# Kernel optimization log

Hardware: AMD Instinct MI355X
Metric: run time of the kernel (lower is better)

The kernel has to match this reference:

```python
import jax, jax.numpy as jnp
import numpy as np

B, T, C, NH = 2, 128, 384, 6
H = 768          # memory MLP hidden (expansion=2)
P, M = 4, 16     # persistent + long-term memory tokens; prefix_len = P+M
LR, MOM, DECAY = 0.01, 0.9, 0.001

def setup_inputs() -> dict:
    key = jax.random.key(0)
    ks = jax.random.split(key, 12)
    s = 0.02
    return {
        'x':          jax.random.normal(ks[0], (B, T, C), jnp.float32),
        'c_attn_w':   jax.random.normal(ks[1], (C, 3 * C), jnp.float32) * s,
        'c_attn_b':   jnp.zeros((3 * C,), jnp.float32),
        'c_proj_w':   jax.random.normal(ks[2], (C, C), jnp.float32) * s,
        'c_proj_b':   jnp.zeros((C,), jnp.float32),
        'ln1_g': jnp.ones((C,), jnp.float32), 'ln1_b': jnp.zeros((C,), jnp.float32),
        'ln2_g': jnp.ones((C,), jnp.float32), 'ln2_b': jnp.zeros((C,), jnp.float32),
        'fc_w':       jax.random.normal(ks[3], (C, 4 * C), jnp.float32) * s,
        'fc_b':       jnp.zeros((4 * C,), jnp.float32),
        'pr_w':       jax.random.normal(ks[4], (4 * C, C), jnp.float32) * s,
        'pr_b':       jnp.zeros((C,), jnp.float32),
        'mem_w1':     jax.random.normal(ks[5], (C, H), jnp.float32) * s,
        'mem_w2':     jax.random.normal(ks[6], (H, C), jnp.float32) * s,
        'wk':         jax.random.normal(ks[7], (C, C), jnp.float32) * s,
        'wv':         jax.random.normal(ks[8], (C, C), jnp.float32) * s,
        'mem_queries': jax.random.normal(ks[9], (M, C), jnp.float32) * s,
        'persist':    jax.random.normal(ks[10], (P, C), jnp.float32) * s,
    }

def _ln(x, g, b):
    mu = jnp.mean(x, -1, keepdims=True)
    var = jnp.mean((x - mu) ** 2, -1, keepdims=True)
    return (x - mu) * jax.lax.rsqrt(var + 1e-5) * g + b

def _scan_log(gates, tokens):
    # x[t] = gate[t]*x[t-1] + token[t] via log-cumsum trick (scan axis = 1)
    while gates.ndim < tokens.ndim:
        gates = gates[..., None]
    g = jnp.clip(gates, 1e-7, 1.0 - 1e-7)
    lc = jnp.cumsum(jnp.log(g), axis=1)
    return jnp.cumsum(tokens * jnp.exp(-lc), axis=1) * jnp.exp(lc)

def _forward(x, c_attn_w, c_attn_b, c_proj_w, c_proj_b, ln1_g, ln1_b, ln2_g, ln2_b,
             fc_w, fc_b, pr_w, pr_b, mem_w1, mem_w2, wk, wv, mem_queries, persist):
    b = x.shape[0]
    hd = C // NH
    PL = P + M
    xn = _ln(x, ln1_g, ln1_b)
    # --- retrieve long-term memory tokens with previous-segment memory weights ---
    retr = jax.nn.silu(mem_queries @ mem_w1) @ mem_w2              # [M, C]
    pref = jnp.concatenate([persist, retr], axis=0)                # [PL, C]
    seq = jnp.concatenate([jnp.broadcast_to(pref, (b, PL, C)), xn], axis=1)  # [b, t, C]
    t = seq.shape[1]
    # --- prefix-LM masked attention ---
    qkv = seq @ c_attn_w + c_attn_b
    q, k, v = jnp.split(qkv, 3, axis=-1)
    def heads(z):
        return z.reshape(b, t, NH, hd).transpose(0, 2, 1, 3)       # [b, nh, t, hd]
    q, k, v = heads(q), heads(k), heads(v)
    sc = jnp.einsum('bhqd,bhkd->bhqk', q, k) / np.float32(np.sqrt(hd))
    idx = jnp.arange(t)
    kp = idx < PL  # key in prefix
    # prefix_lm_mask: key_in_prefix OR (both in suffix AND causal)
    allowed = kp[None, :] | ((~kp[:, None]) & (~kp[None, :]) & (idx[:, None] >= idx[None, :]))
    sc = jnp.where(allowed, sc, -jnp.inf)
    y = jnp.einsum('bhqk,bhkd->bhqd', jax.nn.softmax(sc, axis=-1), v)
    y = y.transpose(0, 2, 1, 3).reshape(b, t, C) @ c_proj_w + c_proj_b
    h1 = x + y[:, PL:, :]                                          # suffix (segment) outputs
    h2n = _ln(h1, ln2_g, ln2_b)
    h2 = h1 + (jax.nn.gelu(h2n @ fc_w + fc_b) @ pr_w + pr_b)
    # --- Titans neural memory update (per-token grads + momentum/decay scans) ---
    km = xn @ wk                                                   # [b, T, C]
    vm = xn @ wv
    hh = km @ mem_w1                                               # [b, T, H]
    a = jax.nn.silu(hh)
    err = a @ mem_w2 - vm                                          # [b, T, C]
    dw2 = jnp.einsum('bth,btc->bthc', a, err)                      # [b, T, H, C]
    sg = jax.nn.sigmoid(hh)
    dh = (err @ mem_w2.T) * (sg * (1.0 + hh * (1.0 - sg)))         # silu'
    dw1 = jnp.einsum('btc,bth->btch', km, dh)                      # [b, T, C, H]
    gm = jnp.full((b, T), MOM, x.dtype)
    scale = -(LR * (1.0 - MOM))
    m1 = _scan_log(gm, scale * dw1)
    m2 = _scan_log(gm, scale * dw2)
    def upd(w0, m):  # W[t] = (1-decay)*W[t-1] + m[t], W[-1] = w0
        toks = jnp.concatenate([jnp.broadcast_to(w0, (b,) + w0.shape)[:, None], m], axis=1)
        g = jnp.concatenate([jnp.ones((b, 1), x.dtype),
                             jnp.full((b, T), 1.0 - DECAY, x.dtype)], axis=1)
        return _scan_log(g, toks)[:, -1]
    w1f = upd(mem_w1, m1)                                          # [b, C, H]
    w2f = upd(mem_w2, m2)                                          # [b, H, C]
    # --- combine block output with updated-memory retrieval ---
    mem_out = jnp.einsum('bth,bhc->btc',
                         jax.nn.silu(jnp.einsum('btc,bch->bth', h2, w1f)), w2f)
    return h2 + mem_out

def reference(x, c_attn_w, c_attn_b, c_proj_w, c_proj_b, ln1_g, ln1_b, ln2_g, ln2_b,
              fc_w, fc_b, pr_w, pr_b, mem_w1, mem_w2, wk, wv, mem_queries, persist):
    return _forward(x, c_attn_w, c_attn_b, c_proj_w, c_proj_b, ln1_g, ln1_b, ln2_g, ln2_b,
                    fc_w, fc_b, pr_w, pr_b, mem_w1, mem_w2, wk, wv, mem_queries, persist)
```

## Files before the change

### kernel.cpp

```cpp
#include <hip/hip_runtime.h>
#include <math.h>

#define B_ 2
#define T_ 128
#define Cc 384
#define NH_ 6
#define HD 64
#define Hh 768
#define P_ 4
#define M_ 16
#define PL_ 20
#define TT 148

typedef unsigned short u16;
typedef short short8 __attribute__((ext_vector_type(8)));
typedef float f32x4 __attribute__((ext_vector_type(4)));

__device__ __forceinline__ u16 f2bf(float f) {
  unsigned int u = __float_as_uint(f);
  u += 0x7FFFu + ((u >> 16) & 1u);
  return (u16)(u >> 16);
}
__device__ __forceinline__ float siluf(float v) { return v / (1.f + expf(-v)); }
__device__ __forceinline__ float geluf(float v) {
  float x3 = v*v*v;
  return 0.5f*v*(1.f + tanhf(0.7978845608028654f*(v + 0.044715f*x3)));
}
template<int ACT> __device__ __forceinline__ float act_apply(float v) {
  if (ACT == 1) return geluf(v);
  if (ACT == 2) return siluf(v);
  return v;
}
__device__ __forceinline__ float coef_f(int k) {
  float e = (float)(T_ - k);
  return (exp2f(e * -0.00144342f) - exp2f(e * -0.15200310f)) * (1.0f/0.099f);
}
__device__ __forceinline__ void st_tr4(u16* dst, float v0, float v1, float v2, float v3) {
  union { u16 u[4]; uint2 d; } q;
  q.u[0]=f2bf(v0); q.u[1]=f2bf(v1); q.u[2]=f2bf(v2); q.u[3]=f2bf(v3);
  *(uint2*)dst = q.d;
}
__device__ __forceinline__ float wave_sum(float s) {
  #pragma unroll
  for (int off = 32; off; off >>= 1) s += __shfl_xor(s, off);
  return s;
}

struct Prm {
  const float *x,*c_attn_w,*c_attn_b,*c_proj_w,*c_proj_b,*ln1_g,*ln1_b,*ln2_g,*ln2_b,
              *fc_w,*fc_b,*pr_w,*pr_b,*mem_w1,*mem_w2,*wk,*wv,*mem_q,*persist;
  float *qkv,*vmb,*h1,*h2,*hhb,*outp;
  u16 *cattnT,*cprojT,*wkT,*wvT,*fcT,*prT,*w1tr,*w2tr,*w2pl,*memq,*hid,*seqb,*yb,*h2n,
      *fco,*h2b,*kmb,*kmTc,*ab,*abTc,*errB,*errT,*dhT,*w1fT,*w2fT,*ub;
  float scale, dpow;
};

template<int KSTEPS>
__device__ __forceinline__ void mfma_core(const u16* __restrict__ A,
    const u16* __restrict__ BT, int M, int mBase, int nBase, float (*red)[64][36])
{
  const long K = (long)KSTEPS * 128;
  int l = threadIdx.x & 63, w = threadIdx.x >> 6;
  int lr = l & 15, kg = l >> 4;
  long r0 = (long)min(mBase + lr, M - 1);
  long r1 = (long)min(mBase + 16 + lr, M - 1);
  long c0 = nBase + lr;
  long ko = (long)w * KSTEPS * 32 + kg * 8;
  const u16* pa0 = A + r0*K + ko;
  const u16* pa1 = A + r1*K + ko;
  const u16* pb0 = BT + c0*K + ko;
  const u16* pb1 = BT + (c0+16)*K + ko;
  const u16* pb2 = BT + (c0+32)*K + ko;
  const u16* pb3 = BT + (c0+48)*K + ko;
  f32x4 acc[2][4] = {};
  short8 a0 = *(const short8*)pa0, a1 = *(const short8*)pa1;
  short8 b0 = *(const short8*)pb0, b1 = *(const short8*)pb1;
  short8 b2 = *(const short8*)pb2, b3 = *(const short8*)pb3;
  #pragma unroll
  for (int t = 0; t < KSTEPS; ++t) {
    short8 xa0=a0, xa1=a1, xb0=b0, xb1=b1, xb2=b2, xb3=b3;
    if (t+1 < KSTEPS) {
      int o = (t+1)*32;
      a0 = *(const short8*)(pa0+o); a1 = *(const short8*)(pa1+o);
      b0 = *(const short8*)(pb0+o); b1 = *(const short8*)(pb1+o);
      b2 = *(const short8*)(pb2+o); b3 = *(const short8*)(pb3+o);
    }
    acc[0][0] = __builtin_amdgcn_mfma_f32_16x16x32_bf16(xa0, xb0, acc[0][0], 0,0,0);
    acc[0][1] = __builtin_amdgcn_mfma_f32_16x16x32_bf16(xa0, xb1, acc[0][1], 0,0,0);
    acc[0][2] = __builtin_amdgcn_mfma_f32_16x16x32_bf16(xa0, xb2, acc[0][2], 0,0,0);
    acc[0][3] = __builtin_amdgcn_mfma_f32_16x16x32_bf16(xa0, xb3, acc[0][3], 0,0,0);
    acc[1][0] = __builtin_amdgcn_mfma_f32_16x16x32_bf16(xa1, xb0, acc[1][0], 0,0,0);
    acc[1][1] = __builtin_amdgcn_mfma_f32_16x16x32_bf16(xa1, xb1, acc[1][1], 0,0,0);
    acc[1][2] = __builtin_amdgcn_mfma_f32_16x16x32_bf16(xa1, xb2, acc[1][2], 0,0,0);
    acc[1][3] = __builtin_amdgcn_mfma_f32_16x16x32_bf16(xa1, xb3, acc[1][3], 0,0,0);
  }
  #pragma unroll
  for (int i = 0; i < 2; ++i)
    #pragma unroll
    for (int j = 0; j < 4; ++j)
      *(f32x4*)&red[w][j*16 + lr][i*16 + kg*4] = acc[i][j];
  __syncthreads();
}

__device__ __forceinline__ void reduce8(float (*red)[64][36], float v[8], int& row0, int& col) {
  int tid = threadIdx.x;
  col = tid & 63;
  row0 = (tid >> 6) * 8;
  #pragma unroll
  for (int q = 0; q < 2; ++q) {
    f32x4 s = *(f32x4*)&red[0][col][row0 + q*4];
    s += *(f32x4*)&red[1][col][row0 + q*4];
    s += *(f32x4*)&red[2][col][row0 + q*4];
    s += *(f32x4*)&red[3][col][row0 + q*4];
    v[q*4+0] = s[0]; v[q*4+1] = s[1]; v[q*4+2] = s[2]; v[q*4+3] = s[3];
  }
}

template<int KSTEPS, int ACT, bool BIAS, bool RES, bool STF, bool STB, bool STTR>
__device__ __forceinline__ void gemm_task(const u16* A, const u16* BT,
    const float* bias, const float* res, float rscale,
    float* outF, u16* outB, u16* outT, int M, int N,
    int xx, int yy, float (*red)[64][36])
{
  int mBase = yy*32, nBase = xx*64;
  mfma_core<KSTEPS>(A, BT, M, mBase, nBase, red);
  float v[8]; int row0, col;
  reduce8(red, v, row0, col);
  int c = nBase + col;
  float bv = BIAS ? bias[c] : 0.f;
  #pragma unroll
  for (int q = 0; q < 8; ++q) {
    int r = mBase + row0 + q;
    float val = act_apply<ACT>(v[q] + bv);
    if (RES && r < M) val += rscale * res[(long)r*N + c];
    v[q] = val;
    if (r < M) {
      if (STF) outF[(long)r*N + c] = val;
      if (STB) outB[(long)r*N + c] = f2bf(val);
    }
  }
  if (STTR) {
    #pragma unroll
    for (int q = 0; q < 2; ++q) {
      int r = mBase + row0 + q*4;
      if (r < M) {
        int zz = r >> 7, t0 = r & 127;
        st_tr4(&outT[((long)zz*N + c)*128 + t0], v[q*4], v[q*4+1], v[q*4+2], v[q*4+3]);
      }
    }
  }
}

__global__ __launch_bounds__(256)
void k0_prep(Prm p)
{
  __shared__ float lds[1056];
  const int t = blockIdx.x;
  const int tid = threadIdx.x, w = tid >> 6, lane = tid & 63;
  if (t < 2592) {
    const float* src; u16* dst; int K, N, tile;
    int b = t;
    if (b < 432)       { src=p.c_attn_w; dst=p.cattnT; K=384;  N=1152; tile=b; }
    else if (b < 576)  { src=p.c_proj_w; dst=p.cprojT; K=384;  N=384;  tile=b-432; }
    else if (b < 720)  { src=p.wk;       dst=p.wkT;    K=384;  N=384;  tile=b-576; }
    else if (b < 864)  { src=p.wv;       dst=p.wvT;    K=384;  N=384;  tile=b-720; }
    else if (b < 1440) { src=p.fc_w;     dst=p.fcT;    K=384;  N=1536; tile=b-864; }
    else if (b < 2016) { src=p.pr_w;     dst=p.prT;    K=1536; N=384;  tile=b-1440; }
    else if (b < 2304) { src=p.mem_w1;   dst=p.w1tr;   K=384;  N=768;  tile=b-2016; }
    else               { src=p.mem_w2;   dst=p.w2tr;   K=768;  N=384;  tile=b-2304; }
    int ntx = N >> 5;
    int n0 = (tile % ntx) << 5, k0 = (tile / ntx) << 5;
    float (*fl)[33] = reinterpret_cast<float(*)[33]>(lds);
    int tr = tid >> 3, tc4 = (tid & 7) << 2;
    float4 vv = *(const float4*)&src[(long)(k0 + tr)*N + n0 + tc4];
    fl[tr][tc4] = vv.x; fl[tr][tc4+1] = vv.y; fl[tr][tc4+2] = vv.z; fl[tr][tc4+3] = vv.w;
    __syncthreads();
    st_tr4(&dst[(long)(n0 + tr)*K + k0 + tc4],
           fl[tc4][tr], fl[tc4+1][tr], fl[tc4+2][tr], fl[tc4+3][tr]);
  } else if (t < 2888) {
    int i = (t - 2592)*256 + tid;
    if (i < 73728) {
      float4 v = *(const float4*)&p.mem_w2[(long)i*4];
      st_tr4(&p.w2pl[(long)i*4], v.x, v.y, v.z, v.w);
    } else if (i < 73728 + 1536) {
      int j = i - 73728;
      float4 v = *(const float4*)&p.mem_q[(long)j*4];
      st_tr4(&p.memq[(long)j*4], v.x, v.y, v.z, v.w);
    } else if (i < 73728 + 1536 + 384) {
      int j = i - 73728 - 1536;
      float4 v = *(const float4*)&p.persist[(long)j*4];
      st_tr4(&p.seqb[(long)j*4], v.x, v.y, v.z, v.w);
      st_tr4(&p.seqb[(long)TT*384 + j*4], v.x, v.y, v.z, v.w);
    }
  } else {
    int row = (t - 2888)*4 + w;
    const float* src = p.x + (long)row*384;
    float v[6];
    #pragma unroll
    for (int i = 0; i < 6; ++i) v[i] = src[lane + i*64];
    float mu = wave_sum(v[0]+v[1]+v[2]+v[3]+v[4]+v[5]) * (1.f/384.f);
    float sq = 0.f;
    #pragma unroll
    for (int i = 0; i < 6; ++i) { float d = v[i]-mu; sq += d*d; }
    float rstd = rsqrtf(wave_sum(sq)*(1.f/384.f) + 1e-5f);
    u16* dst = p.seqb + ((long)(row >> 7)*TT + PL_ + (row & 127))*384;
    #pragma unroll
    for (int i = 0; i < 6; ++i) {
      int cc = lane + i*64;
      dst[cc] = f2bf((v[i]-mu)*rstd*p.ln1_g[cc] + p.ln1_b[cc]);
    }
  }
}

__global__ __launch_bounds__(256, 2)
void k0b_hid(Prm p)
{
  __shared__ float red[4][64][36];
  gemm_task<3,2,false,false,false,true,false>(p.memq, p.w1tr, nullptr, nullptr, 0.f,
      nullptr, p.hid, nullptr, 16, 768, blockIdx.x, 0, red);
}

__global__ __launch_bounds__(256, 2)
void k0c_retr(Prm p)
{
  __shared__ float red[4][64][36];
  int nBase = blockIdx.x*64;
  mfma_core<6>(p.hid, p.w2tr, 16, 0, nBase, red);
  float v[8]; int row0, col;
  reduce8(red, v, row0, col);
  int c = nBase + col;
  #pragma unroll
  for (int q = 0; q < 8; ++q) {
    int r = row0 + q;
    if (r < 16) {
      u16 bv = f2bf(v[q]);
      p.seqb[(long)(P_ + r)*384 + c] = bv;
      p.seqb[(long)(TT + P_ + r)*384 + c] = bv;
    }
  }
}

__global__ __launch_bounds__(256, 2)
void k1_qkv(Prm p)
{
  __shared__ float red[4][64][36];
  int t = blockIdx.x;
  int xx = t % 30, yy = t / 30;
  int nb = xx * 64;
  const u16* BT; int n0, seg;
  if (nb < 1152)      { BT = p.cattnT; n0 = nb;        seg = 0; }
  else if (nb < 1536) { BT = p.wkT;    n0 = nb - 1152; seg = 1; }
  else                { BT = p.wvT;    n0 = nb - 1536; seg = 2; }
  int mBase = yy*32;
  mfma_core<3>(p.seqb, BT, 296, mBase, n0, red);
  float v[8]; int row0, col;
  reduce8(red, v, row0, col);
  int c = n0 + col;
  if (seg == 0) {
    float bv = p.c_attn_b[c];
    #pragma unroll
    for (int q = 0; q < 8; ++q) {
      int r = mBase + row0 + q;
      if (r < 296) p.qkv[(long)r*1152 + c] = v[q] + bv;
    }
  } else if (seg == 1) {
    #pragma unroll
    for (int q = 0; q < 8; ++q) {
      int r = mBase + row0 + q;
      if (r < 296) {
        int z = r/148, tt2 = r - 20 - z*148;
        if (tt2 >= 0) p.kmb[((long)z*128 + tt2)*384 + c] = f2bf(v[q]);
      }
    }
    #pragma unroll
    for (int q = 0; q < 2; ++q) {
      int r = mBase + row0 + q*4;
      if (r < 296) {
        int z = r/148, t0 = r - 20 - z*148;
        if (t0 >= 0)
          st_tr4(&p.kmTc[((long)z*384 + c)*128 + t0],
                 v[q*4]*coef_f(t0), v[q*4+1]*coef_f(t0+1),
                 v[q*4+2]*coef_f(t0+2), v[q*4+3]*coef_f(t0+3));
      }
    }
  } else {
    #pragma unroll
    for (int q = 0; q < 8; ++q) {
      int r = mBase + row0 + q;
      if (r < 296) {
        int z = r/148, tt2 = r - 20 - z*148;
        if (tt2 >= 0) p.vmb[((long)z*128 + tt2)*384 + c] = v[q];
      }
    }
  }
}

__global__ __launch_bounds__(256)
void k2_attn(Prm p)
{
  __shared__ float qs4[4][64];
  __shared__ float pp4[4][152];
  const int tid = threadIdx.x, w = tid >> 6, lane = tid & 63;
  int t = blockIdx.x*4 + w;
  int qr = PL_ + (t & 127);
  int h  = (t >> 7) % 6;
  int b  = (t / 768) & 1;
  const float* base = p.qkv + (long)b*TT*1152;
  float* qs = qs4[w];
  float* pp = pp4[w];
  qs[lane] = base[(long)qr*1152 + h*64 + lane];
  float mloc = -1e30f;
  for (int k = lane; k < TT; k += 64) {
    float s = -1e30f;
    if (k <= qr) {
      const float* kp = base + (long)k*1152 + 384 + h*64;
      float acc = 0.f;
      #pragma unroll
      for (int d = 0; d < 64; ++d) acc += qs[d]*kp[d];
      s = acc * 0.125f;
    }
    pp[k] = s;
    mloc = fmaxf(mloc, s);
  }
  #pragma unroll
  for (int off = 32; off; off >>= 1) mloc = fmaxf(mloc, __shfl_xor(mloc, off));
  float ssum = 0.f;
  for (int k = lane; k < TT; k += 64) {
    float e = (k <= qr) ? expf(pp[k] - mloc) : 0.f;
    pp[k] = e; ssum += e;
  }
  ssum = wave_sum(ssum);
  float inv = 1.f / ssum;
  float acc = 0.f;
  const float* vb = base + 768 + h*64 + lane;
  int k = 0;
  for (; k + 4 <= qr + 1; k += 4)
    acc += pp[k]*vb[(long)k*1152] + pp[k+1]*vb[(long)(k+1)*1152]
         + pp[k+2]*vb[(long)(k+2)*1152] + pp[k+3]*vb[(long)(k+3)*1152];
  for (; k <= qr; ++k) acc += pp[k]*vb[(long)k*1152];
  p.yb[((long)b*128 + (t & 127))*384 + h*64 + lane] = f2bf(acc * inv);
}

__global__ __launch_bounds__(256, 2)
void k3_h1hh(Prm p)
{
  __shared__ float red[4][64][36];
  int t = blockIdx.x;
  if (t < 48) {
    gemm_task<3,0,true,true,true,false,false>(p.yb, p.cprojT, p.c_proj_b, p.x, 1.f,
        p.h1, nullptr, nullptr, 256, 384, t % 6, t / 6, red);
  } else {
    int tt2 = t - 48;
    int xx = tt2 % 12, yy = tt2 / 12;
    int mBase = yy*32, nBase = xx*64;
    mfma_core<3>(p.kmb, p.w1tr, 256, mBase, nBase, red);
    float v[8]; int row0, col;
    reduce8(red, v, row0, col);
    int c = nBase + col;
    float s8[8];
    #pragma unroll
    for (int q = 0; q < 8; ++q) {
      int r = mBase + row0 + q;
      p.hhb[(long)r*768 + c] = v[q];
      s8[q] = siluf(v[q]);
      p.ab[(long)r*768 + c] = f2bf(s8[q]);
    }
    #pragma unroll
    for (int q = 0; q < 2; ++q) {
      int r = mBase + row0 + q*4;
      int zz = r >> 7, t0 = r & 127;
      st_tr4(&p.abTc[((long)zz*768 + c)*128 + t0],
             s8[q*4]*coef_f(t0), s8[q*4+1]*coef_f(t0+1),
             s8[q*4+2]*coef_f(t0+2), s8[q*4+3]*coef_f(t0+3));
    }
  }
}

__global__ __launch_bounds__(256, 2)
void k4_ln2err(Prm p)
{
  __shared__ float red[4][64][36];
  int t = blockIdx.x;
  const int tid = threadIdx.x, w = tid >> 6, lane = tid & 63;
  if (t < 64) {
    int row = t*4 + w;
    const float* src = p.h1 + (long)row*384;
    float v[6];
    #pragma unroll
    for (int i = 0; i < 6; ++i) v[i] = src[lane + i*64];
    float mu = wave_sum(v[0]+v[1]+v[2]+v[3]+v[4]+v[5]) * (1.f/384.f);
    float sq = 0.f;
    #pragma unroll
    for (int i = 0; i < 6; ++i) { float d = v[i]-mu; sq += d*d; }
    float rstd = rsqrtf(wave_sum(sq)*(1.f/384.f) + 1e-5f);
    u16* dst = p.h2n + (long)row*384;
    #pragma unroll
    for (int i = 0; i < 6; ++i) {
      int cc = lane + i*64;
      dst[cc] = f2bf((v[i]-mu)*rstd*p.ln2_g[cc] + p.ln2_b[cc]);
    }
  } else {
    int tt2 = t - 64;
    gemm_task<6,0,false,true,false,true,true>(p.ab, p.w2tr, nullptr, p.vmb, -1.f,
        nullptr, p.errB, p.errT, 256, 384, tt2 % 6, tt2 / 6, red);
  }
}

__global__ __launch_bounds__(256, 2)
void k5_fcodh(Prm p)
{
  __shared__ float red[4][64][36];
  int t = blockIdx.x;
  if (t < 192) {
    gemm_task<3,1,true,false,false,true,false>(p.h2n, p.fcT, p.fc_b, nullptr, 0.f,
        nullptr, p.fco, nullptr, 256, 1536, t % 24, t / 24, red);
  } else {
    int tt2 = t - 192;
    int xx = tt2 % 12, yy = tt2 / 12;
    int mBase = yy*32, nBase = xx*64;
    mfma_core<3>(p.errB, p.w2pl, 256, mBase, nBase, red);
    float v[8]; int row0, col;
    reduce8(red, v, row0, col);
    int c = nBase + col;
    #pragma unroll
    for (int q = 0; q < 8; ++q) {
      int r = mBase + row0 + q;
      float h = p.hhb[(long)r*768 + c];
      float sg = 1.f/(1.f + expf(-h));
      v[q] = v[q] * (sg*(1.f + h*(1.f - sg)));
    }
    #pragma unroll
    for (int q = 0; q < 2; ++q) {
      int r = mBase + row0 + q*4;
      int zz = r >> 7, t0 = r & 127;
      st_tr4(&p.dhT[((long)zz*768 + c)*128 + t0], v[q*4], v[q*4+1], v[q*4+2], v[q*4+3]);
    }
  }
}

__global__ __launch_bounds__(256, 2)
void k6_h2wupd(Prm p)
{
  __shared__ float red[4][64][36];
  int t = blockIdx.x;
  if (t < 48) {
    gemm_task<12,0,true,true,true,true,false>(p.fco, p.prT, p.pr_b, p.h1, 1.f,
        p.h2, p.h2b, nullptr, 256, 384, t % 6, t / 6, red);
  } else {
    const u16 *A, *BT; const float* W0; u16* Oz; int M, N, xx, yy, z;
    if (t < 336) {
      int tt2 = t - 48;
      xx = tt2 % 12; yy = (tt2 / 12) % 12; z = tt2 / 144;
      M = 384; N = 768;
      A = p.kmTc + (long)z*M*128; BT = p.dhT + (long)z*N*128;
      W0 = p.mem_w1; Oz = p.w1fT + (long)z*M*N;
    } else {
      int tt2 = t - 336;
      xx = tt2 % 6; yy = (tt2 / 6) % 24; z = tt2 / 144;
      M = 768; N = 384;
      A = p.abTc + (long)z*M*128; BT = p.errT + (long)z*N*128;
      W0 = p.mem_w2; Oz = p.w2fT + (long)z*M*N;
    }
    int mBase = yy*32, nBase = xx*64;
    mfma_core<1>(A, BT, M, mBase, nBase, red);
    float v[8]; int row0, col;
    reduce8(red, v, row0, col);
    int c = nBase + col;
    #pragma unroll
    for (int q = 0; q < 8; ++q) {
      int r = mBase + row0 + q;
      v[q] = p.dpow*W0[(long)r*N + c] + p.scale*v[q];
    }
    int r0 = mBase + row0;
    st_tr4(&Oz[(long)c*M + r0],     v[0], v[1], v[2], v[3]);
    st_tr4(&Oz[(long)c*M + r0 + 4], v[4], v[5], v[6], v[7]);
  }
}

__global__ __launch_bounds__(256, 2)
void k7_ub(Prm p)
{
  __shared__ float red[4][64][36];
  int t = blockIdx.x;
  int z = t / 48, rr = t % 48;
  gemm_task<3,2,false,false,false,true,false>(
      p.h2b + (long)z*128*384, p.w1fT + (long)z*768*384, nullptr, nullptr, 0.f,
      nullptr, p.ub + (long)z*128*768, nullptr, 128, 768, rr % 12, rr / 12, red);
}

__global__ __launch_bounds__(256, 2)
void k8_out(Prm p)
{
  __shared__ float red[4][64][36];
  int t = blockIdx.x;
  int z = t / 24, rr = t % 24;
  gemm_task<6,0,false,true,true,false,false>(
      p.ub + (long)z*128*768, p.w2fT + (long)z*384*768, nullptr,
      p.h2 + (long)z*128*384, 1.f,
      p.outp + (long)z*128*384, nullptr, nullptr, 128, 384, rr % 6, rr / 6, red);
}

extern "C" void kernel_launch(void* const* d_in, const int* in_sizes, int n_in,
                              void* d_out, int out_size, void* d_ws, size_t ws_size,
                              hipStream_t stream)
{
  Prm p;
  p.x        = (const float*)d_in[0];
  p.c_attn_w = (const float*)d_in[1];
  p.c_attn_b = (const float*)d_in[2];
  p.c_proj_w = (const float*)d_in[3];
  p.c_proj_b = (const float*)d_in[4];
  p.ln1_g    = (const float*)d_in[5];
  p.ln1_b    = (const float*)d_in[6];
  p.ln2_g    = (const float*)d_in[7];
  p.ln2_b    = (const float*)d_in[8];
  p.fc_w     = (const float*)d_in[9];
  p.fc_b     = (const float*)d_in[10];
  p.pr_w     = (const float*)d_in[11];
  p.pr_b     = (const float*)d_in[12];
  p.mem_w1   = (const float*)d_in[13];
  p.mem_w2   = (const float*)d_in[14];
  p.wk       = (const float*)d_in[15];
  p.wv       = (const float*)d_in[16];
  p.mem_q    = (const float*)d_in[17];
  p.persist  = (const float*)d_in[18];

  float* f = (float*)d_ws;
  p.qkv = f;            f += 296L*1152;
  p.vmb = f;            f += 256L*384;
  p.h1  = f;            f += 256L*384;
  p.h2  = f;            f += 256L*384;
  p.hhb = f;            f += 256L*768;
  u16* b = (u16*)f;
  p.cattnT = b;  b += 1152L*384;
  p.cprojT = b;  b += 384L*384;
  p.wkT    = b;  b += 384L*384;
  p.wvT    = b;  b += 384L*384;
  p.fcT    = b;  b += 1536L*384;
  p.prT    = b;  b += 384L*1536;
  p.w1tr   = b;  b += 768L*384;
  p.w2tr   = b;  b += 384L*768;
  p.w2pl   = b;  b += 768L*384;
  p.memq   = b;  b += 16L*384;
  p.hid    = b;  b += 16L*768;
  p.seqb   = b;  b += 2L*TT*384;
  p.yb     = b;  b += 256L*384;
  p.h2n    = b;  b += 256L*384;
  p.fco    = b;  b += 256L*1536;
  p.h2b    = b;  b += 256L*384;
  p.kmb    = b;  b += 256L*384;
  p.kmTc   = b;  b += 2L*384*128;
  p.ab     = b;  b += 256L*768;
  p.abTc   = b;  b += 2L*768*128;
  p.errB   = b;  b += 256L*384;
  p.errT   = b;  b += 2L*384*128;
  p.dhT    = b;  b += 2L*768*128;
  p.w1fT   = b;  b += 2L*768*384;
  p.w2fT   = b;  b += 2L*384*768;
  p.ub     = b;  b += 2L*128*768;
  p.outp   = (float*)d_out;
  p.dpow   = powf(0.999f, 128.f);
  p.scale  = -0.001f;

  hipLaunchKernelGGL(k0_prep,   dim3(2952), dim3(256), 0, stream, p);
  hipLaunchKernelGGL(k0b_hid,   dim3(12),   dim3(256), 0, stream, p);
  hipLaunchKernelGGL(k0c_retr,  dim3(6),    dim3(256), 0, stream, p);
  hipLaunchKernelGGL(k1_qkv,    dim3(300),  dim3(256), 0, stream, p);
  hipLaunchKernelGGL(k2_attn,   dim3(384),  dim3(256), 0, stream, p);
  hipLaunchKernelGGL(k3_h1hh,   dim3(144),  dim3(256), 0, stream, p);
  hipLaunchKernelGGL(k4_ln2err, dim3(112),  dim3(256), 0, stream, p);
  hipLaunchKernelGGL(k5_fcodh,  dim3(288),  dim3(256), 0, stream, p);
  hipLaunchKernelGGL(k6_h2wupd, dim3(624),  dim3(256), 0, stream, p);
  hipLaunchKernelGGL(k7_ub,     dim3(96),   dim3(256), 0, stream, p);
  hipLaunchKernelGGL(k8_out,    dim3(48),   dim3(256), 0, stream, p);
}
```

Baseline: 99.04 us.

## Regroup independent stages into fewer launches and fuse memory hidden into retrieval

The kernel that computes the memory-query hidden layer is folded into the retrieval kernel. Each of its 6 blocks recomputes the full 16x768 hidden activation into LDS, which removes one launch and a global round trip. The later stages are regrouped so that independent work shares a launch: attention runs with the hh GEMM, c_proj with the error GEMM, LN2 with dh, and fc with the weight updates. The final h2 projection gets its own small launch. This drops one launch and its barrier and gives small GEMMs more co-resident work, at the cost of redundant hidden computation, lower occupancy in the retrieval kernel, and mixed block types within a launch.

Result: slower. 123.5 us (+24.7%).

```diff
diff --git a/kernel.cpp b/kernel.cpp
--- a/kernel.cpp
+++ b/kernel.cpp
@@ -50,7 +50,7 @@
   const float *x,*c_attn_w,*c_attn_b,*c_proj_w,*c_proj_b,*ln1_g,*ln1_b,*ln2_g,*ln2_b,
               *fc_w,*fc_b,*pr_w,*pr_b,*mem_w1,*mem_w2,*wk,*wv,*mem_q,*persist;
   float *qkv,*vmb,*h1,*h2,*hhb,*outp;
-  u16 *cattnT,*cprojT,*wkT,*wvT,*fcT,*prT,*w1tr,*w2tr,*w2pl,*memq,*hid,*seqb,*yb,*h2n,
+  u16 *cattnT,*cprojT,*wkT,*wvT,*fcT,*prT,*w1tr,*w2tr,*w2pl,*memq,*seqb,*yb,*h2n,
       *fco,*h2b,*kmb,*kmTc,*ab,*abTc,*errB,*errT,*dhT,*w1fT,*w2fT,*ub;
   float scale, dpow;
 };
@@ -212,20 +212,25 @@
   }
 }
 
-__global__ __launch_bounds__(256, 2)
-void k0b_hid(Prm p)
-{
-  __shared__ float red[4][64][36];
-  gemm_task<3,2,false,false,false,true,false>(p.memq, p.w1tr, nullptr, nullptr, 0.f,
-      nullptr, p.hid, nullptr, 16, 768, blockIdx.x, 0, red);
-}
-
-__global__ __launch_bounds__(256, 2)
+__global__ __launch_bounds__(256, 1)
 void k0c_retr(Prm p)
 {
   __shared__ float red[4][64][36];
+  __shared__ u16 hidl[16*768];
+  for (int xx = 0; xx < 12; ++xx) {
+    mfma_core<3>(p.memq, p.w1tr, 16, 0, xx*64, red);
+    float v[8]; int row0, col;
+    reduce8(red, v, row0, col);
+    int c = xx*64 + col;
+    #pragma unroll
+    for (int q = 0; q < 8; ++q) {
+      int r = row0 + q;
+      if (r < 16) hidl[r*768 + c] = f2bf(siluf(v[q]));
+    }
+    __syncthreads();
+  }
   int nBase = blockIdx.x*64;
-  mfma_core<6>(p.hid, p.w2tr, 16, 0, nBase, red);
+  mfma_core<6>((const u16*)hidl, p.w2tr, 16, 0, nBase, red);
   float v[8]; int row0, col;
   reduce8(red, v, row0, col);
   int c = nBase + col;
@@ -295,62 +300,54 @@
   }
 }
 
-__global__ __launch_bounds__(256)
-void k2_attn(Prm p)
-{
-  __shared__ float qs4[4][64];
-  __shared__ float pp4[4][152];
+__global__ __launch_bounds__(256, 2)
+void k2_attn_hh(Prm p)
+{
+  __shared__ float red[4][64][36];
+  const int t = blockIdx.x;
   const int tid = threadIdx.x, w = tid >> 6, lane = tid & 63;
-  int t = blockIdx.x*4 + w;
-  int qr = PL_ + (t & 127);
-  int h  = (t >> 7) % 6;
-  int b  = (t / 768) & 1;
-  const float* base = p.qkv + (long)b*TT*1152;
-  float* qs = qs4[w];
-  float* pp = pp4[w];
-  qs[lane] = base[(long)qr*1152 + h*64 + lane];
-  float mloc = -1e30f;
-  for (int k = lane; k < TT; k += 64) {
-    float s = -1e30f;
-    if (k <= qr) {
-      const float* kp = base + (long)k*1152 + 384 + h*64;
-      float acc = 0.f;
-      #pragma unroll
-      for (int d = 0; d < 64; ++d) acc += qs[d]*kp[d];
-      s = acc * 0.125f;
-    }
-    pp[k] = s;
-    mloc = fmaxf(mloc, s);
-  }
-  #pragma unroll
-  for (int off = 32; off; off >>= 1) mloc = fmaxf(mloc, __shfl_xor(mloc, off));
-  float ssum = 0.f;
-  for (int k = lane; k < TT; k += 64) {
-    float e = (k <= qr) ? expf(pp[k] - mloc) : 0.f;
-    pp[k] = e; ssum += e;
-  }
-  ssum = wave_sum(ssum);
-  float inv = 1.f / ssum;
-  float acc = 0.f;
-  const float* vb = base + 768 + h*64 + lane;
-  int k = 0;
-  for (; k + 4 <= qr + 1; k += 4)
-    acc += pp[k]*vb[(long)k*1152] + pp[k+1]*vb[(long)(k+1)*1152]
-         + pp[k+2]*vb[(long)(k+2)*1152] + pp[k+3]*vb[(long)(k+3)*1152];
-  for (; k <= qr; ++k) acc += pp[k]*vb[(long)k*1152];
-  p.yb[((long)b*128 + (t & 127))*384 + h*64 + lane] = f2bf(acc * inv);
-}
-
-__global__ __launch_bounds__(256, 2)
-void k3_h1hh(Prm p)
-{
-  __shared__ float red[4][64][36];
-  int t = blockIdx.x;
-  if (t < 48) {
-    gemm_task<3,0,true,true,true,false,false>(p.yb, p.cprojT, p.c_proj_b, p.x, 1.f,
-        p.h1, nullptr, nullptr, 256, 384, t % 6, t / 6, red);
+  if (t < 384) {
+    float* ldsf = (float*)red;
+    float* qs = ldsf + w*64;
+    float* pp = ldsf + 256 + w*152;
+    int tt = t*4 + w;
+    int qr = PL_ + (tt & 127);
+    int h  = (tt >> 7) % 6;
+    int b  = (tt / 768) & 1;
+    const float* base = p.qkv + (long)b*TT*1152;
+    qs[lane] = base[(long)qr*1152 + h*64 + lane];
+    float mloc = -1e30f;
+    for (int k = lane; k < TT; k += 64) {
+      float s = -1e30f;
+      if (k <= qr) {
+        const float* kp = base + (long)k*1152 + 384 + h*64;
+        float acc = 0.f;
+        #pragma unroll
+        for (int d = 0; d < 64; ++d) acc += qs[d]*kp[d];
+        s = acc * 0.125f;
+      }
+      pp[k] = s;
+      mloc = fmaxf(mloc, s);
+    }
+    #pragma unroll
+    for (int off = 32; off; off >>= 1) mloc = fmaxf(mloc, __shfl_xor(mloc, off));
+    float ssum = 0.f;
+    for (int k = lane; k < TT; k += 64) {
+      float e = (k <= qr) ? expf(pp[k] - mloc) : 0.f;
+      pp[k] = e; ssum += e;
+    }
+    ssum = wave_sum(ssum);
+    float inv = 1.f / ssum;
+    float acc = 0.f;
+    const float* vb = base + 768 + h*64 + lane;
+    int k = 0;
+    for (; k + 4 <= qr + 1; k += 4)
+      acc += pp[k]*vb[(long)k*1152] + pp[k+1]*vb[(long)(k+1)*1152]
+           + pp[k+2]*vb[(long)(k+2)*1152] + pp[k+3]*vb[(long)(k+3)*1152];
+    for (; k <= qr; ++k) acc += pp[k]*vb[(long)k*1152];
+    p.yb[((long)b*128 + (tt & 127))*384 + h*64 + lane] = f2bf(acc * inv);
   } else {
-    int tt2 = t - 48;
+    int tt2 = t - 384;
     int xx = tt2 % 12, yy = tt2 / 12;
     int mBase = yy*32, nBase = xx*64;
     mfma_core<3>(p.kmb, p.w1tr, 256, mBase, nBase, red);
@@ -377,7 +374,22 @@
 }
 
 __global__ __launch_bounds__(256, 2)
-void k4_ln2err(Prm p)
+void k3_h1err(Prm p)
+{
+  __shared__ float red[4][64][36];
+  int t = blockIdx.x;
+  if (t < 48) {
+    gemm_task<3,0,true,true,true,false,false>(p.yb, p.cprojT, p.c_proj_b, p.x, 1.f,
+        p.h1, nullptr, nullptr, 256, 384, t % 6, t / 6, red);
+  } else {
+    int tt2 = t - 48;
+    gemm_task<6,0,false,true,false,true,true>(p.ab, p.w2tr, nullptr, p.vmb, -1.f,
+        nullptr, p.errB, p.errT, 256, 384, tt2 % 6, tt2 / 6, red);
+  }
+}
+
+__global__ __launch_bounds__(256, 2)
+void k4_ln2dh(Prm p)
 {
   __shared__ float red[4][64][36];
   int t = blockIdx.x;
@@ -401,21 +413,6 @@
     }
   } else {
     int tt2 = t - 64;
-    gemm_task<6,0,false,true,false,true,true>(p.ab, p.w2tr, nullptr, p.vmb, -1.f,
-        nullptr, p.errB, p.errT, 256, 384, tt2 % 6, tt2 / 6, red);
-  }
-}
-
-__global__ __launch_bounds__(256, 2)
-void k5_fcodh(Prm p)
-{
-  __shared__ float red[4][64][36];
-  int t = blockIdx.x;
-  if (t < 192) {
-    gemm_task<3,1,true,false,false,true,false>(p.h2n, p.fcT, p.fc_b, nullptr, 0.f,
-        nullptr, p.fco, nullptr, 256, 1536, t % 24, t / 24, red);
-  } else {
-    int tt2 = t - 192;
     int xx = tt2 % 12, yy = tt2 / 12;
     int mBase = yy*32, nBase = xx*64;
     mfma_core<3>(p.errB, p.w2pl, 256, mBase, nBase, red);
@@ -439,23 +436,23 @@
 }
 
 __global__ __launch_bounds__(256, 2)
-void k6_h2wupd(Prm p)
-{
-  __shared__ float red[4][64][36];
-  int t = blockIdx.x;
-  if (t < 48) {
-    gemm_task<12,0,true,true,true,true,false>(p.fco, p.prT, p.pr_b, p.h1, 1.f,
-        p.h2, p.h2b, nullptr, 256, 384, t % 6, t / 6, red);
+void k5_fcowupd(Prm p)
+{
+  __shared__ float red[4][64][36];
+  int t = blockIdx.x;
+  if (t < 192) {
+    gemm_task<3,1,true,false,false,true,false>(p.h2n, p.fcT, p.fc_b, nullptr, 0.f,
+        nullptr, p.fco, nullptr, 256, 1536, t % 24, t / 24, red);
   } else {
     const u16 *A, *BT; const float* W0; u16* Oz; int M, N, xx, yy, z;
-    if (t < 336) {
-      int tt2 = t - 48;
+    if (t < 480) {
+      int tt2 = t - 192;
       xx = tt2 % 12; yy = (tt2 / 12) % 12; z = tt2 / 144;
       M = 384; N = 768;
       A = p.kmTc + (long)z*M*128; BT = p.dhT + (long)z*N*128;
       W0 = p.mem_w1; Oz = p.w1fT + (long)z*M*N;
     } else {
-      int tt2 = t - 336;
+      int tt2 = t - 480;
       xx = tt2 % 6; yy = (tt2 / 6) % 24; z = tt2 / 144;
       M = 768; N = 384;
       A = p.abTc + (long)z*M*128; BT = p.errT + (long)z*N*128;
@@ -475,6 +472,15 @@
     st_tr4(&Oz[(long)c*M + r0],     v[0], v[1], v[2], v[3]);
     st_tr4(&Oz[(long)c*M + r0 + 4], v[4], v[5], v[6], v[7]);
   }
+}
+
+__global__ __launch_bounds__(256, 2)
+void k6_h2(Prm p)
+{
+  __shared__ float red[4][64][36];
+  int t = blockIdx.x;
+  gemm_task<12,0,true,true,true,true,false>(p.fco, p.prT, p.pr_b, p.h1, 1.f,
+      p.h2, p.h2b, nullptr, 256, 384, t % 6, t / 6, red);
 }
 
 __global__ __launch_bounds__(256, 2)
@@ -542,7 +548,6 @@
   p.w2tr   = b;  b += 384L*768;
   p.w2pl   = b;  b += 768L*384;
   p.memq   = b;  b += 16L*384;
-  p.hid    = b;  b += 16L*768;
   p.seqb   = b;  b += 2L*TT*384;
   p.yb     = b;  b += 256L*384;
   p.h2n    = b;  b += 256L*384;
@@ -562,15 +567,14 @@
   p.dpow   = powf(0.999f, 128.f);
   p.scale  = -0.001f;
 
-  hipLaunchKernelGGL(k0_prep,   dim3(2952), dim3(256), 0, stream, p);
-  hipLaunchKernelGGL(k0b_hid,   dim3(12),   dim3(256), 0, stream, p);
-  hipLaunchKernelGGL(k0c_retr,  dim3(6),    dim3(256), 0, stream, p);
-  hipLaunchKernelGGL(k1_qkv,    dim3(300),  dim3(256), 0, stream, p);
-  hipLaunchKernelGGL(k2_attn,   dim3(384),  dim3(256), 0, stream, p);
-  hipLaunchKernelGGL(k3_h1hh,   dim3(144),  dim3(256), 0, stream, p);
-  hipLaunchKernelGGL(k4_ln2err, dim3(112),  dim3(256), 0, stream, p);
-  hipLaunchKernelGGL(k5_fcodh,  dim3(288),  dim3(256), 0, stream, p);
-  hipLaunchKernelGGL(k6_h2wupd, dim3(624),  dim3(256), 0, stream, p);
-  hipLaunchKernelGGL(k7_ub,     dim3(96),   dim3(256), 0, stream, p);
-  hipLaunchKernelGGL(k8_out,    dim3(48),   dim3(256), 0, stream, p);
-}
+  hipLaunchKernelGGL(k0_prep,    dim3(2952), dim3(256), 0, stream, p);
+  hipLaunchKernelGGL(k0c_retr,   dim3(6),    dim3(256), 0, stream, p);
+  hipLaunchKernelGGL(k1_qkv,     dim3(300),  dim3(256), 0, stream, p);
+  hipLaunchKernelGGL(k2_attn_hh, dim3(480),  dim3(256), 0, stream, p);
+  hipLaunchKernelGGL(k3_h1err,   dim3(96),   dim3(256), 0, stream, p);
+  hipLaunchKernelGGL(k4_ln2dh,   dim3(160),  dim3(256), 0, stream, p);
+  hipLaunchKernelGGL(k5_fcowupd, dim3(768),  dim3(256), 0, stream, p);
+  hipLaunchKernelGGL(k6_h2,      dim3(48),   dim3(256), 0, stream, p);
+  hipLaunchKernelGGL(k7_ub,      dim3(96),   dim3(256), 0, stream, p);
+  hipLaunchKernelGGL(k8_out,     dim3(48),   dim3(256), 0, stream, p);
+}
```
